# Optimization experiments

Hardware: AMD Instinct MI355X
Metric: run time of the kernel (lower is better)

Reference implementation:

```python
import jax, jax.numpy as jnp
import numpy as np

KE_KCAL = 332.0636  # Coulomb constant, kcal/mol * Angstrom / e^2
R_CUT = 5.0
R_ON = R_CUT / 4.0
R_OFF = 3.0 * R_CUT / 4.0
B, A, F = 32, 1024, 128  # molecules, atoms per molecule, feature dim
MAX_Z = 86


def silu(x):
    return x * jax.nn.sigmoid(x)


def res_mlp(x, W1, W2, Wout):
    # Residual (two pre-activation linears) -> activation -> Linear, no biases
    h = silu(x) @ W1
    h = silu(h) @ W2
    return silu(x + h) @ Wout


def f_switch(r):
    # smooth switching function built from sigma(x)=exp(-1/x) for x>0 else 0
    arg = (r - R_ON) / (R_OFF - R_ON)
    def sigma(x):
        xs = jnp.where(x > 0, x, 1.0)
        return jnp.where(x > 0, jnp.exp(-1.0 / xs), 0.0)
    num = sigma(1.0 - arg)
    return num / (num + sigma(arg))


def setup_inputs() -> dict:
    key = jax.random.key(0)
    ks = jax.random.split(key, 16)
    box = 22.0  # ~liquid density box for 1024 atoms (Angstrom)
    s = 1.0 / np.sqrt(F)
    return {
        'e_z': jax.random.normal(ks[0], (B * A, F), jnp.float32) * 0.1,
        'charge': jax.random.normal(ks[1], (B,), jnp.float32),
        'xyz': jax.random.uniform(ks[2], (B, A, 3), jnp.float32) * box,
        'W_lin': jax.random.normal(ks[3], (F, F), jnp.float32) * s,
        'b_lin': jnp.zeros((F,), jnp.float32),
        'k_plus': jax.random.normal(ks[4], (F,), jnp.float32) * s,
        'k_minus': jax.random.normal(ks[5], (F,), jnp.float32) * s,
        'v_plus': jax.random.normal(ks[6], (F,), jnp.float32) * s,
        'v_minus': jax.random.normal(ks[7], (F,), jnp.float32) * s,
        'Wr1': jax.random.normal(ks[8], (F, F), jnp.float32) * s,
        'Wr2': jax.random.normal(ks[9], (F, F), jnp.float32) * s,
        'Wout': jax.random.normal(ks[10], (F, F), jnp.float32) * s,
        'w_e': jax.random.normal(ks[11], (F,), jnp.float32) * s,
        'q_z_table': jax.random.normal(ks[12], (MAX_Z,), jnp.float32) * 0.01,
        'z': jax.random.randint(ks[13], (B * A,), 1, MAX_Z, jnp.int32),
    }


def reference(e_z, charge, xyz, W_lin, b_lin, k_plus, k_minus, v_plus, v_minus,
              Wr1, Wr2, Wout, w_e, q_z_table, z):
    # ---- ElectronicEmbedding (per-molecule loop vectorized over B) ----
    q = (e_z @ W_lin + b_lin).reshape(B, A, F)
    pos = (charge >= 0)[:, None]                       # [B,1]
    k = jnp.where(pos, k_plus[None, :], k_minus[None, :])   # [B,F]
    v = jnp.where(pos, v_plus[None, :], v_minus[None, :])   # [B,F]
    arg = jnp.einsum('baf,bf->ba', q, k) / np.sqrt(F)
    num = jax.nn.softplus(arg)                         # log(1+exp)
    a = charge[:, None] * num / num.sum(axis=1, keepdims=True)  # [B,A]
    av = a[:, :, None] * v[:, None, :]                 # [B,A,F]
    e_psi = res_mlp(av.reshape(B * A, F), Wr1, Wr2, Wout)
    f = e_z + e_psi                                    # atom features [N,F]

    # ---- Electrostatics.get_charge (charge-conserving correction) ----
    pred_q = (f @ w_e + q_z_table[z]).reshape(B, A)
    corr = (charge - pred_q.sum(axis=1)) / A
    q_atom = pred_q + corr[:, None]                    # [B,A]

    # ---- Electrostatics.get_en: O(A^2) pairwise switched Coulomb ----
    diff = xyz[:, :, None, :] - xyz[:, None, :, :]     # [B,A,A,3]
    r2 = jnp.sum(diff * diff, axis=-1)                 # [B,A,A]
    mask = jnp.triu(jnp.ones((A, A), bool), k=1)       # pairs j > i (r>0)
    r = jnp.sqrt(jnp.where(mask, r2, 1.0))
    fs = f_switch(r)
    coul = fs / jnp.sqrt(r * r + 1.0) + (1.0 - fs) / r
    pair_e = q_atom[:, :, None] * q_atom[:, None, :] * coul
    energy = KE_KCAL * jnp.sum(jnp.where(mask, pair_e, 0.0), axis=(1, 2))  # [B]
    return energy
```

## Files before the change

### kernel.cpp

```cpp
#include <hip/hip_runtime.h>
#include <math.h>

#define B_MOL 32
#define A_AT  1024
#define NF    128
#define N_AT  (B_MOL * A_AT)

#define WS_NUMSUM   512
#define WS_PREDSUM  544
#define WS_PRED     16384
#define WS_SIDX     49152
#define WS_SPOS     81920
#define WS_CTR      214528

typedef short short8 __attribute__((ext_vector_type(8)));
typedef float floatx4 __attribute__((ext_vector_type(4)));

__device__ __forceinline__ float fast_rcp(float x) { return __builtin_amdgcn_rcpf(x); }
__device__ __forceinline__ float fast_rsq(float x) { return __builtin_amdgcn_rsqf(x); }
__device__ __forceinline__ float silu_f(float x) { return x * fast_rcp(1.f + __expf(-x)); }

__device__ __forceinline__ short f2bf(float x) {
  unsigned u = __float_as_uint(x);
  u += 0x7fffu + ((u >> 16) & 1u);
  return (short)(u >> 16);
}

__device__ __forceinline__ float wave_sum(float v) {
#pragma unroll
  for (int o = 32; o > 0; o >>= 1) v += __shfl_xor(v, o, 64);
  return v;
}

__global__ __launch_bounds__(256, 2) void attn_mlp_kernel(
    const float* __restrict__ e_z, const float* __restrict__ charge,
    const float* __restrict__ xyz, const float* __restrict__ W_lin,
    const float* __restrict__ b_lin, const float* __restrict__ k_plus,
    const float* __restrict__ k_minus, const float* __restrict__ v_plus,
    const float* __restrict__ v_minus, const float* __restrict__ Wr1,
    const float* __restrict__ Wr2, const float* __restrict__ Wout,
    const float* __restrict__ w_e, const float* __restrict__ qz_table,
    const int* __restrict__ z, float* __restrict__ ws) {
  int bx = blockIdx.x, tid = threadIdx.x;
  int mol = bx >> 4, s = bx & 15;
  int base = bx * 64;

  __shared__ __align__(16) char big[50176];
  __shared__ float num_sh[64], ezwe_sh[64], wout_sh[128], awsh[64], vsh[128];
  __shared__ float cc_sh, bsum_sh;

  float* k2 = (float*)big;
  float* wesh = k2 + 128;
  int* hist = (int*)(wesh + 128);
  int* startc = hist + 64;
  float* numred = (float*)(startc + 64);
  unsigned* ctr = (unsigned*)(ws + WS_CTR) + mol * 16;

  float ch = charge[mol];
  bool cpos = ch >= 0.f;
  const float* kvec = cpos ? k_plus : k_minus;

  {
    int r = tid & 127;
    const float* M = (tid < 128) ? W_lin : Wout;
    const float* vv = (tid < 128) ? kvec : w_e;
    const float4* row = (const float4*)(M + (size_t)r * NF);
    float acc = 0.f;
#pragma unroll 8
    for (int i = 0; i < 32; i++) {
      float4 a = row[i];
      float4 b = ((const float4*)vv)[i];
      acc = fmaf(a.x, b.x, acc); acc = fmaf(a.y, b.y, acc);
      acc = fmaf(a.z, b.z, acc); acc = fmaf(a.w, b.w, acc);
    }
    if (tid < 128) { k2[r] = acc; wesh[r] = w_e[r]; }
    else wout_sh[r] = acc;
  }
  if (tid < 64) {
    float c = b_lin[tid] * kvec[tid] + b_lin[tid + 64] * kvec[tid + 64];
    c = wave_sum(c);
    if (tid == 0) cc_sh = c;
  }
  __syncthreads();

  int w = tid >> 6, l = tid & 63, half = l >> 5, l31 = l & 31;
  {
    int b4 = l31 * 4;
    float ka = k2[b4], kb = k2[b4 + 1], kc = k2[b4 + 2], kd = k2[b4 + 3];
    float wa = wesh[b4], wb = wesh[b4 + 1], wc = wesh[b4 + 2], wd = wesh[b4 + 3];
    float cc = cc_sh;
    float wavenum = 0.f;
#pragma unroll
    for (int it = 0; it < 8; it++) {
      int m = it * 8 + w * 2 + half;
      int n = base + m;
      float4 v = *((const float4*)(e_z + (size_t)n * NF) + l31);
      float dk = v.x * ka; dk = fmaf(v.y, kb, dk); dk = fmaf(v.z, kc, dk); dk = fmaf(v.w, kd, dk);
      float dw = v.x * wa; dw = fmaf(v.y, wb, dw); dw = fmaf(v.z, wc, dw); dw = fmaf(v.w, wd, dw);
#pragma unroll
      for (int o = 1; o < 32; o <<= 1) {
        dk += __shfl_xor(dk, o, 64);
        dw += __shfl_xor(dw, o, 64);
      }
      if (l31 == 0) {
        float arg = (dk + cc) * 0.08838834764831845f;
        float num = fmaxf(arg, 0.f) + log1pf(__expf(-fabsf(arg)));
        num_sh[m] = num;
        ezwe_sh[m] = dw;
        wavenum += num;
      }
    }
    wavenum += __shfl_xor(wavenum, 32, 64);
    if (l == 0) numred[w] = wavenum;
  }
  __syncthreads();
  if (tid == 0)
    atomicAdd(&ws[WS_NUMSUM + mol], numred[0] + numred[1] + numred[2] + numred[3]);

  if (s == 0) {
    if (tid < 64) hist[tid] = 0;
    __syncthreads();
    float px[4], py[4], pz[4];
    int cell[4];
#pragma unroll
    for (int r = 0; r < 4; r++) {
      int j = tid + r * 256;
      const float* p = xyz + (size_t)(mol * A_AT + j) * 3;
      px[r] = p[0]; py[r] = p[1]; pz[r] = p[2];
      int cx = min(3, max(0, (int)(px[r] * (4.f / 22.f))));
      int cy = min(3, max(0, (int)(py[r] * (4.f / 22.f))));
      int cz = min(3, max(0, (int)(pz[r] * (4.f / 22.f))));
      cell[r] = cx * 16 + cy * 4 + cz;
      atomicAdd(&hist[cell[r]], 1);
    }
    __syncthreads();
    if (tid == 0) {
      int acc = 0;
      for (int c = 0; c < 64; c++) { startc[c] = acc; acc += hist[c]; }
    }
    __syncthreads();
    float4* spos = (float4*)(ws + WS_SPOS);
    int* sidx = (int*)(ws + WS_SIDX);
#pragma unroll
    for (int r = 0; r < 4; r++) {
      int j = tid + r * 256;
      int off = atomicAdd(&startc[cell[r]], 1);
      int g = mol * A_AT + off;
      spos[g] = make_float4(px[r], py[r], pz[r], 0.f);
      sidx[g] = j;
    }
  }

  __syncthreads();
  if (tid == 0) {
    __hip_atomic_fetch_add(ctr, 1u, __ATOMIC_RELAXED, __HIP_MEMORY_SCOPE_AGENT);
    while (__hip_atomic_fetch_add(ctr, 0u, __ATOMIC_RELAXED,
                                  __HIP_MEMORY_SCOPE_AGENT) < 16u)
      __builtin_amdgcn_s_sleep(8);
    bsum_sh = __hip_atomic_fetch_add(&ws[WS_NUMSUM + mol], 0.0f,
                                     __ATOMIC_RELAXED, __HIP_MEMORY_SCOPE_AGENT);
  }
  if (tid < 128) vsh[tid] = cpos ? v_plus[tid] : v_minus[tid];
  __syncthreads();
  if (tid < 64) awsh[tid] = ch * num_sh[tid] / bsum_sh;

  short* wf = (short*)big;
  short* a2s = (short*)(big + 32768);
#pragma unroll
  for (int e = 0; e < 8; e++) {
    int idx = e * 256 + tid;
    int fi = idx >> 6, ln = idx & 63;
    int nt = fi >> 2, ks = fi & 3;
    const float* src = Wr1 + (size_t)(ks * 32 + (ln >> 4) * 8) * NF + nt * 16 + (ln & 15);
    short8 v;
#pragma unroll
    for (int j = 0; j < 8; j++) v[j] = f2bf(src[j * NF]);
    *(short8*)&wf[idx * 8] = v;
  }
  __syncthreads();

  int q = l >> 4, l15 = l & 15;
  float aw_m = awsh[w * 16 + l15];
  floatx4 acc1[8];
#pragma unroll
  for (int nt = 0; nt < 8; nt++) acc1[nt] = (floatx4)(0.f);

#pragma unroll
  for (int ks = 0; ks < 4; ks++) {
    float4 va = *(const float4*)&vsh[ks * 32 + q * 8];
    float4 vb = *(const float4*)&vsh[ks * 32 + q * 8 + 4];
    short8 af;
    af[0] = f2bf(silu_f(aw_m * va.x)); af[1] = f2bf(silu_f(aw_m * va.y));
    af[2] = f2bf(silu_f(aw_m * va.z)); af[3] = f2bf(silu_f(aw_m * va.w));
    af[4] = f2bf(silu_f(aw_m * vb.x)); af[5] = f2bf(silu_f(aw_m * vb.y));
    af[6] = f2bf(silu_f(aw_m * vb.z)); af[7] = f2bf(silu_f(aw_m * vb.w));
#pragma unroll
    for (int nt = 0; nt < 8; nt++) {
      short8 bf = *(const short8*)&wf[(nt * 4 + ks) * 512 + l * 8];
      acc1[nt] = __builtin_amdgcn_mfma_f32_16x16x32_bf16(af, bf, acc1[nt], 0, 0, 0);
    }
  }

#pragma unroll
  for (int nt = 0; nt < 8; nt++) {
    int f = nt * 16 + l15;
#pragma unroll
    for (int r = 0; r < 4; r++)
      a2s[w * 2176 + (q * 4 + r) * 136 + f] = f2bf(silu_f(acc1[nt][r]));
  }
  __syncthreads();
#pragma unroll
  for (int e = 0; e < 8; e++) {
    int idx = e * 256 + tid;
    int fi = idx >> 6, ln = idx & 63;
    int nt = fi >> 2, ks = fi & 3;
    const float* src = Wr2 + (size_t)(ks * 32 + (ln >> 4) * 8) * NF + nt * 16 + (ln & 15);
    short8 v;
#pragma unroll
    for (int j = 0; j < 8; j++) v[j] = f2bf(src[j * NF]);
    *(short8*)&wf[idx * 8] = v;
  }
  __syncthreads();

  floatx4 acc2[8];
#pragma unroll
  for (int nt = 0; nt < 8; nt++) acc2[nt] = (floatx4)(0.f);

#pragma unroll
  for (int ks = 0; ks < 4; ks++) {
    short8 af = *(const short8*)&a2s[w * 2176 + l15 * 136 + ks * 32 + q * 8];
#pragma unroll
    for (int nt = 0; nt < 8; nt++) {
      short8 bf = *(const short8*)&wf[(nt * 4 + ks) * 512 + l * 8];
      acc2[nt] = __builtin_amdgcn_mfma_f32_16x16x32_bf16(af, bf, acc2[nt], 0, 0, 0);
    }
  }

  float awq[4], part[4];
#pragma unroll
  for (int r = 0; r < 4; r++) {
    awq[r] = awsh[w * 16 + q * 4 + r];
    part[r] = 0.f;
  }
#pragma unroll
  for (int nt = 0; nt < 8; nt++) {
    int f = nt * 16 + l15;
    float vv = vsh[f], ww2 = wout_sh[f];
#pragma unroll
    for (int r = 0; r < 4; r++) {
      float sfl = silu_f(fmaf(awq[r], vv, acc2[nt][r]));
      part[r] = fmaf(sfl, ww2, part[r]);
    }
  }
#pragma unroll
  for (int r = 0; r < 4; r++) {
#pragma unroll
    for (int o = 1; o < 16; o <<= 1) part[r] += __shfl_xor(part[r], o, 64);
  }
  float* pred_shf = (float*)(big + 32768);
  __syncthreads();
  if (l15 == 0) {
#pragma unroll
    for (int r = 0; r < 4; r++) {
      int m = w * 16 + q * 4 + r;
      int n = base + m;
      float pred = part[r] + ezwe_sh[m] + qz_table[z[n]];
      ws[WS_PRED + n] = pred;
      pred_shf[m] = pred;
    }
  }
  __syncthreads();
  if (tid < 64) {
    float ssum = wave_sum(pred_shf[tid]);
    if (tid == 0) atomicAdd(&ws[WS_PREDSUM + mol], ssum);
  }
}

__global__ __launch_bounds__(256) void pair_kernel(const float* __restrict__ charge,
                                                   float* __restrict__ ws,
                                                   float* __restrict__ out) {
  int bx = blockIdx.x;
  int mol = bx >> 4;
  int s = bx & 15;
  int tid = threadIdx.x;
  int w = tid >> 6, lane = tid & 63;
  __shared__ float4 posq[1024];
  __shared__ float wred[4];
  const float4* spos = (const float4*)(ws + WS_SPOS);
  const int* sidx = (const int*)(ws + WS_SIDX);
  float corr = (charge[mol] - ws[WS_PREDSUM + mol]) * (1.f / 1024.f);
  for (int j = tid; j < 1024; j += 256) {
    float4 p = spos[mol * 1024 + j];
    p.w = ws[WS_PRED + mol * 1024 + sidx[mol * 1024 + j]] + corr;
    posq[j] = p;
  }
  __syncthreads();
  int i = s * 64 + lane;
  float4 me = posq[i];
  float e = 0.f;
  for (int c = s + w; c < 16; c += 4) {
    int j0 = c * 64;
    if (c == s) {
#pragma unroll 4
      for (int j = j0; j < j0 + 64; j++) {
        float4 p = posq[j];
        float dx = me.x - p.x, dy = me.y - p.y, dz = me.z - p.z;
        float r2 = fmaf(dx, dx, fmaf(dy, dy, dz * dz));
        bool skip = (j <= i);
        float r2s = skip ? 1.0e8f : r2;
        float qj = skip ? 0.f : p.w;
        float inv_r = fast_rsq(r2s);
        e = fmaf(qj, inv_r, e);
        if (__any(r2s < 14.0625f)) {
          float r = r2s * inv_r;
          float arg = (r - 1.25f) * 0.4f;
          float argc = fminf(fmaxf(arg, 1e-6f), 1.f - 1e-6f);
          float t = fast_rcp(argc) - fast_rcp(1.f - argc);
          float fs = fast_rcp(1.f + __expf(-t));
          float delta = fs * (fast_rsq(r2s + 1.f) - inv_r);
          e = fmaf(qj, delta, e);
        }
      }
    } else {
#pragma unroll 4
      for (int j = j0; j < j0 + 64; j++) {
        float4 p = posq[j];
        float dx = me.x - p.x, dy = me.y - p.y, dz = me.z - p.z;
        float r2 = fmaf(dx, dx, fmaf(dy, dy, dz * dz));
        float qj = p.w;
        float inv_r = fast_rsq(r2);
        e = fmaf(qj, inv_r, e);
        if (__any(r2 < 14.0625f)) {
          float r = r2 * inv_r;
          float arg = (r - 1.25f) * 0.4f;
          float argc = fminf(fmaxf(arg, 1e-6f), 1.f - 1e-6f);
          float t = fast_rcp(argc) - fast_rcp(1.f - argc);
          float fs = fast_rcp(1.f + __expf(-t));
          float delta = fs * (fast_rsq(r2 + 1.f) - inv_r);
          e = fmaf(qj, delta, e);
        }
      }
    }
  }
  e *= me.w;
  float sred = wave_sum(e);
  if (lane == 0) wred[w] = sred;
  __syncthreads();
  if (tid == 0)
    atomicAdd(&out[mol], 332.0636f * (wred[0] + wred[1] + wred[2] + wred[3]));
}

extern "C" void kernel_launch(void* const* d_in, const int* in_sizes, int n_in,
                              void* d_out, int out_size, void* d_ws, size_t ws_size,
                              hipStream_t stream) {
  const float* e_z     = (const float*)d_in[0];
  const float* charge  = (const float*)d_in[1];
  const float* xyz     = (const float*)d_in[2];
  const float* W_lin   = (const float*)d_in[3];
  const float* b_lin   = (const float*)d_in[4];
  const float* k_plus  = (const float*)d_in[5];
  const float* k_minus = (const float*)d_in[6];
  const float* v_plus  = (const float*)d_in[7];
  const float* v_minus = (const float*)d_in[8];
  const float* Wr1     = (const float*)d_in[9];
  const float* Wr2     = (const float*)d_in[10];
  const float* Wout    = (const float*)d_in[11];
  const float* w_e     = (const float*)d_in[12];
  const float* qz      = (const float*)d_in[13];
  const int*   z       = (const int*)d_in[14];
  float* out = (float*)d_out;
  float* ws  = (float*)d_ws;

  hipMemsetAsync(ws + WS_NUMSUM, 0, 64 * sizeof(float), stream);
  hipMemsetAsync(ws + WS_CTR, 0, 512 * sizeof(unsigned), stream);
  hipMemsetAsync(out, 0, B_MOL * sizeof(float), stream);
  attn_mlp_kernel<<<512, 256, 0, stream>>>(e_z, charge, xyz, W_lin, b_lin,
                                           k_plus, k_minus, v_plus, v_minus,
                                           Wr1, Wr2, Wout, w_e, qz, z, ws);
  pair_kernel<<<512, 256, 0, stream>>>(charge, ws, out);
}
```

Baseline: 154.3 us.

## Split fused attention/MLP kernel into three launches, drop spin barrier and memsets

Replaces the intra-kernel grid spin-wait (per-molecule counter plus atomic num-sum) with a kernel boundary. A new first kernel computes softplus numerators, sorts atoms into cells and pre-converts Wr1/Wr2 into bf16 MFMA fragment layout once. An MLP kernel then copies those fragments from global memory instead of converting per block. The three memsets are removed (out is zeroed inside the first kernel, sums are recomputed locally), and the pair kernel balances its triangular block work with a rotated chunk schedule. This adds a launch and extra global round-trips for intermediates.

```diff
diff --git a/kernel.cpp b/kernel.cpp
--- a/kernel.cpp
+++ b/kernel.cpp
@@ -6,12 +6,14 @@
 #define NF    128
 #define N_AT  (B_MOL * A_AT)
 
-#define WS_NUMSUM   512
-#define WS_PREDSUM  544
-#define WS_PRED     16384
-#define WS_SIDX     49152
-#define WS_SPOS     81920
-#define WS_CTR      214528
+#define WS_FRAG1    0
+#define WS_FRAG2    8192
+#define WS_WOUT     16384
+#define WS_NUM      16512
+#define WS_EZWE     49280
+#define WS_PREDS    82048
+#define WS_IINV     114816
+#define WS_SPOS     147584
 
 typedef short short8 __attribute__((ext_vector_type(8)));
 typedef float floatx4 __attribute__((ext_vector_type(4)));
@@ -32,49 +34,37 @@
   return v;
 }
 
-__global__ __launch_bounds__(256, 2) void attn_mlp_kernel(
+__global__ __launch_bounds__(256) void attn_sort_kernel(
     const float* __restrict__ e_z, const float* __restrict__ charge,
     const float* __restrict__ xyz, const float* __restrict__ W_lin,
     const float* __restrict__ b_lin, const float* __restrict__ k_plus,
-    const float* __restrict__ k_minus, const float* __restrict__ v_plus,
-    const float* __restrict__ v_minus, const float* __restrict__ Wr1,
+    const float* __restrict__ k_minus, const float* __restrict__ Wr1,
     const float* __restrict__ Wr2, const float* __restrict__ Wout,
-    const float* __restrict__ w_e, const float* __restrict__ qz_table,
-    const int* __restrict__ z, float* __restrict__ ws) {
+    const float* __restrict__ w_e, float* __restrict__ ws,
+    float* __restrict__ out) {
   int bx = blockIdx.x, tid = threadIdx.x;
   int mol = bx >> 4, s = bx & 15;
   int base = bx * 64;
 
-  __shared__ __align__(16) char big[50176];
-  __shared__ float num_sh[64], ezwe_sh[64], wout_sh[128], awsh[64], vsh[128];
-  __shared__ float cc_sh, bsum_sh;
-
-  float* k2 = (float*)big;
-  float* wesh = k2 + 128;
-  int* hist = (int*)(wesh + 128);
-  int* startc = hist + 64;
-  float* numred = (float*)(startc + 64);
-  unsigned* ctr = (unsigned*)(ws + WS_CTR) + mol * 16;
+  __shared__ float k2[NF], wesh[NF];
+  __shared__ int hist[64], startc[64];
+  __shared__ float cc_sh;
 
   float ch = charge[mol];
-  bool cpos = ch >= 0.f;
-  const float* kvec = cpos ? k_plus : k_minus;
-
-  {
-    int r = tid & 127;
-    const float* M = (tid < 128) ? W_lin : Wout;
-    const float* vv = (tid < 128) ? kvec : w_e;
-    const float4* row = (const float4*)(M + (size_t)r * NF);
+  const float* kvec = (ch >= 0.f) ? k_plus : k_minus;
+
+  if (tid < 128) {
+    const float4* row = (const float4*)(W_lin + (size_t)tid * NF);
     float acc = 0.f;
 #pragma unroll 8
     for (int i = 0; i < 32; i++) {
       float4 a = row[i];
-      float4 b = ((const float4*)vv)[i];
+      float4 b = ((const float4*)kvec)[i];
       acc = fmaf(a.x, b.x, acc); acc = fmaf(a.y, b.y, acc);
       acc = fmaf(a.z, b.z, acc); acc = fmaf(a.w, b.w, acc);
     }
-    if (tid < 128) { k2[r] = acc; wesh[r] = w_e[r]; }
-    else wout_sh[r] = acc;
+    k2[tid] = acc;
+    wesh[tid] = w_e[tid];
   }
   if (tid < 64) {
     float c = b_lin[tid] * kvec[tid] + b_lin[tid + 64] * kvec[tid + 64];
@@ -89,7 +79,6 @@
     float ka = k2[b4], kb = k2[b4 + 1], kc = k2[b4 + 2], kd = k2[b4 + 3];
     float wa = wesh[b4], wb = wesh[b4 + 1], wc = wesh[b4 + 2], wd = wesh[b4 + 3];
     float cc = cc_sh;
-    float wavenum = 0.f;
 #pragma unroll
     for (int it = 0; it < 8; it++) {
       int m = it * 8 + w * 2 + half;
@@ -104,18 +93,11 @@
       }
       if (l31 == 0) {
         float arg = (dk + cc) * 0.08838834764831845f;
-        float num = fmaxf(arg, 0.f) + log1pf(__expf(-fabsf(arg)));
-        num_sh[m] = num;
-        ezwe_sh[m] = dw;
-        wavenum += num;
-      }
-    }
-    wavenum += __shfl_xor(wavenum, 32, 64);
-    if (l == 0) numred[w] = wavenum;
-  }
-  __syncthreads();
-  if (tid == 0)
-    atomicAdd(&ws[WS_NUMSUM + mol], numred[0] + numred[1] + numred[2] + numred[3]);
+        ws[WS_NUM + n] = fmaxf(arg, 0.f) + log1pf(__expf(-fabsf(arg)));
+        ws[WS_EZWE + n] = dw;
+      }
+    }
+  }
 
   if (s == 0) {
     if (tid < 64) hist[tid] = 0;
@@ -140,42 +122,80 @@
     }
     __syncthreads();
     float4* spos = (float4*)(ws + WS_SPOS);
-    int* sidx = (int*)(ws + WS_SIDX);
+    int* iinv = (int*)ws + WS_IINV;
 #pragma unroll
     for (int r = 0; r < 4; r++) {
       int j = tid + r * 256;
       int off = atomicAdd(&startc[cell[r]], 1);
-      int g = mol * A_AT + off;
-      spos[g] = make_float4(px[r], py[r], pz[r], 0.f);
-      sidx[g] = j;
-    }
-  }
-
-  __syncthreads();
-  if (tid == 0) {
-    __hip_atomic_fetch_add(ctr, 1u, __ATOMIC_RELAXED, __HIP_MEMORY_SCOPE_AGENT);
-    while (__hip_atomic_fetch_add(ctr, 0u, __ATOMIC_RELAXED,
-                                  __HIP_MEMORY_SCOPE_AGENT) < 16u)
-      __builtin_amdgcn_s_sleep(8);
-    bsum_sh = __hip_atomic_fetch_add(&ws[WS_NUMSUM + mol], 0.0f,
-                                     __ATOMIC_RELAXED, __HIP_MEMORY_SCOPE_AGENT);
-  }
-  if (tid < 128) vsh[tid] = cpos ? v_plus[tid] : v_minus[tid];
-  __syncthreads();
-  if (tid < 64) awsh[tid] = ch * num_sh[tid] / bsum_sh;
-
-  short* wf = (short*)big;
-  short* a2s = (short*)(big + 32768);
-#pragma unroll
-  for (int e = 0; e < 8; e++) {
-    int idx = e * 256 + tid;
-    int fi = idx >> 6, ln = idx & 63;
-    int nt = fi >> 2, ks = fi & 3;
-    const float* src = Wr1 + (size_t)(ks * 32 + (ln >> 4) * 8) * NF + nt * 16 + (ln & 15);
-    short8 v;
-#pragma unroll
-    for (int j = 0; j < 8; j++) v[j] = f2bf(src[j * NF]);
-    *(short8*)&wf[idx * 8] = v;
+      spos[mol * A_AT + off] = make_float4(px[r], py[r], pz[r], 0.f);
+      iinv[mol * A_AT + j] = mol * A_AT + off;
+    }
+  } else if (mol == 0 && (s == 1 || s == 2)) {
+    const float* W = (s == 1) ? Wr1 : Wr2;
+    short* dst = (short*)(ws + ((s == 1) ? WS_FRAG1 : WS_FRAG2));
+#pragma unroll
+    for (int it = 0; it < 16; it++) {
+      int idx = it * 256 + tid;
+      int k = idx >> 5;
+      int c0 = (idx & 31) * 4;
+      float4 v = ((const float4*)W)[idx];
+      int ks = k >> 5, q = (k & 31) >> 3, j = k & 7;
+      float vv[4] = {v.x, v.y, v.z, v.w};
+#pragma unroll
+      for (int e = 0; e < 4; e++) {
+        int col = c0 + e;
+        int fi = (col >> 4) * 4 + ks;
+        int lane = q * 16 + (col & 15);
+        dst[fi * 512 + lane * 8 + j] = f2bf(vv[e]);
+      }
+    }
+  } else if (mol == 0 && s == 3) {
+    if (tid < 128) {
+      float sw = 0.f;
+      for (int f = 0; f < NF; f++) sw = fmaf(Wout[tid * NF + f], w_e[f], sw);
+      ws[WS_WOUT + tid] = sw;
+    }
+    if (tid >= 128 && tid < 160) out[tid - 128] = 0.f;
+  }
+}
+
+__global__ __launch_bounds__(256) void mlp_kernel(
+    const float* __restrict__ charge, const float* __restrict__ v_plus,
+    const float* __restrict__ v_minus, const int* __restrict__ z,
+    const float* __restrict__ qz_table, float* __restrict__ ws) {
+  int bx = blockIdx.x, tid = threadIdx.x;
+  int mol = bx >> 4;
+  int base = bx * 64;
+  int w = tid >> 6, l = tid & 63;
+
+  __shared__ __align__(16) short wf[16384];
+  __shared__ short a2s[4 * 16 * 136];
+  __shared__ float vsh[NF], wout_sh[NF], awsh[64], ezwe_sh[64], wred[4];
+  __shared__ float numsum_sh;
+
+  float ch = charge[mol];
+  {
+    float4 nv = ((const float4*)(ws + WS_NUM + mol * A_AT))[tid];
+    float p = nv.x + nv.y + nv.z + nv.w;
+    p = wave_sum(p);
+    if (l == 0) wred[w] = p;
+  }
+  if (tid < 128) {
+    vsh[tid] = (ch >= 0.f) ? v_plus[tid] : v_minus[tid];
+    wout_sh[tid] = ws[WS_WOUT + tid];
+  }
+  {
+    const float4* src = (const float4*)(ws + WS_FRAG1);
+    float4* dst = (float4*)wf;
+#pragma unroll
+    for (int r = 0; r < 8; r++) dst[tid + r * 256] = src[tid + r * 256];
+  }
+  __syncthreads();
+  if (tid == 0) numsum_sh = wred[0] + wred[1] + wred[2] + wred[3];
+  __syncthreads();
+  if (tid < 64) {
+    awsh[tid] = ch * ws[WS_NUM + base + tid] / numsum_sh;
+    ezwe_sh[tid] = ws[WS_EZWE + base + tid];
   }
   __syncthreads();
 
@@ -209,16 +229,11 @@
       a2s[w * 2176 + (q * 4 + r) * 136 + f] = f2bf(silu_f(acc1[nt][r]));
   }
   __syncthreads();
-#pragma unroll
-  for (int e = 0; e < 8; e++) {
-    int idx = e * 256 + tid;
-    int fi = idx >> 6, ln = idx & 63;
-    int nt = fi >> 2, ks = fi & 3;
-    const float* src = Wr2 + (size_t)(ks * 32 + (ln >> 4) * 8) * NF + nt * 16 + (ln & 15);
-    short8 v;
-#pragma unroll
-    for (int j = 0; j < 8; j++) v[j] = f2bf(src[j * NF]);
-    *(short8*)&wf[idx * 8] = v;
+  {
+    const float4* src = (const float4*)(ws + WS_FRAG2);
+    float4* dst = (float4*)wf;
+#pragma unroll
+    for (int r = 0; r < 8; r++) dst[tid + r * 256] = src[tid + r * 256];
   }
   __syncthreads();
 
@@ -257,50 +272,52 @@
 #pragma unroll
     for (int o = 1; o < 16; o <<= 1) part[r] += __shfl_xor(part[r], o, 64);
   }
-  float* pred_shf = (float*)(big + 32768);
-  __syncthreads();
   if (l15 == 0) {
+    const int* iinv = (const int*)ws + WS_IINV;
 #pragma unroll
     for (int r = 0; r < 4; r++) {
       int m = w * 16 + q * 4 + r;
       int n = base + m;
-      float pred = part[r] + ezwe_sh[m] + qz_table[z[n]];
-      ws[WS_PRED + n] = pred;
-      pred_shf[m] = pred;
-    }
-  }
-  __syncthreads();
-  if (tid < 64) {
-    float ssum = wave_sum(pred_shf[tid]);
-    if (tid == 0) atomicAdd(&ws[WS_PREDSUM + mol], ssum);
+      ws[WS_PREDS + iinv[n]] = part[r] + ezwe_sh[m] + qz_table[z[n]];
+    }
   }
 }
 
 __global__ __launch_bounds__(256) void pair_kernel(const float* __restrict__ charge,
-                                                   float* __restrict__ ws,
+                                                   const float* __restrict__ ws,
                                                    float* __restrict__ out) {
   int bx = blockIdx.x;
   int mol = bx >> 4;
-  int s = bx & 15;
+  int a = bx & 15;
   int tid = threadIdx.x;
-  int w = tid >> 6, lane = tid & 63;
+  int w = tid >> 6, l = tid & 63;
   __shared__ float4 posq[1024];
   __shared__ float wred[4];
   const float4* spos = (const float4*)(ws + WS_SPOS);
-  const int* sidx = (const int*)(ws + WS_SIDX);
-  float corr = (charge[mol] - ws[WS_PREDSUM + mol]) * (1.f / 1024.f);
+  const float* preds = ws + WS_PREDS + mol * A_AT;
+  float psum = 0.f;
   for (int j = tid; j < 1024; j += 256) {
-    float4 p = spos[mol * 1024 + j];
-    p.w = ws[WS_PRED + mol * 1024 + sidx[mol * 1024 + j]] + corr;
+    float4 p = spos[mol * A_AT + j];
+    p.w = preds[j];
     posq[j] = p;
-  }
-  __syncthreads();
-  int i = s * 64 + lane;
+    psum += p.w;
+  }
+  psum = wave_sum(psum);
+  if (l == 0) wred[w] = psum;
+  __syncthreads();
+  float corr = (charge[mol] - (wred[0] + wred[1] + wred[2] + wred[3])) * (1.f / 1024.f);
+  for (int j = tid; j < 1024; j += 256) posq[j].w += corr;
+  __syncthreads();
+
+  int i = a * 64 + l;
   float4 me = posq[i];
   float e = 0.f;
-  for (int c = s + w; c < 16; c += 4) {
+#pragma unroll
+  for (int t = 0; t < 2; t++) {
+    int d = w + t * 4;
+    int c = (a + d) & 15;
     int j0 = c * 64;
-    if (c == s) {
+    if (d == 0) {
 #pragma unroll 4
       for (int j = j0; j < j0 + 64; j++) {
         float4 p = posq[j];
@@ -315,8 +332,8 @@
           float r = r2s * inv_r;
           float arg = (r - 1.25f) * 0.4f;
           float argc = fminf(fmaxf(arg, 1e-6f), 1.f - 1e-6f);
-          float t = fast_rcp(argc) - fast_rcp(1.f - argc);
-          float fs = fast_rcp(1.f + __expf(-t));
+          float tt = fast_rcp(argc) - fast_rcp(1.f - argc);
+          float fs = fast_rcp(1.f + __expf(-tt));
           float delta = fs * (fast_rsq(r2s + 1.f) - inv_r);
           e = fmaf(qj, delta, e);
         }
@@ -334,17 +351,38 @@
           float r = r2 * inv_r;
           float arg = (r - 1.25f) * 0.4f;
           float argc = fminf(fmaxf(arg, 1e-6f), 1.f - 1e-6f);
-          float t = fast_rcp(argc) - fast_rcp(1.f - argc);
-          float fs = fast_rcp(1.f + __expf(-t));
+          float tt = fast_rcp(argc) - fast_rcp(1.f - argc);
+          float fs = fast_rcp(1.f + __expf(-tt));
           float delta = fs * (fast_rsq(r2 + 1.f) - inv_r);
           e = fmaf(qj, delta, e);
         }
       }
     }
   }
+  if (a < 8 && w == (a & 3)) {
+    int j0 = ((a + 8) & 15) * 64;
+#pragma unroll 4
+    for (int j = j0; j < j0 + 64; j++) {
+      float4 p = posq[j];
+      float dx = me.x - p.x, dy = me.y - p.y, dz = me.z - p.z;
+      float r2 = fmaf(dx, dx, fmaf(dy, dy, dz * dz));
+      float qj = p.w;
+      float inv_r = fast_rsq(r2);
+      e = fmaf(qj, inv_r, e);
+      if (__any(r2 < 14.0625f)) {
+        float r = r2 * inv_r;
+        float arg = (r - 1.25f) * 0.4f;
+        float argc = fminf(fmaxf(arg, 1e-6f), 1.f - 1e-6f);
+        float tt = fast_rcp(argc) - fast_rcp(1.f - argc);
+        float fs = fast_rcp(1.f + __expf(-tt));
+        float delta = fs * (fast_rsq(r2 + 1.f) - inv_r);
+        e = fmaf(qj, delta, e);
+      }
+    }
+  }
   e *= me.w;
   float sred = wave_sum(e);
-  if (lane == 0) wred[w] = sred;
+  if (l == 0) wred[w] = sred;
   __syncthreads();
   if (tid == 0)
     atomicAdd(&out[mol], 332.0636f * (wred[0] + wred[1] + wred[2] + wred[3]));
@@ -371,11 +409,9 @@
   float* out = (float*)d_out;
   float* ws  = (float*)d_ws;
 
-  hipMemsetAsync(ws + WS_NUMSUM, 0, 64 * sizeof(float), stream);
-  hipMemsetAsync(ws + WS_CTR, 0, 512 * sizeof(unsigned), stream);
-  hipMemsetAsync(out, 0, B_MOL * sizeof(float), stream);
-  attn_mlp_kernel<<<512, 256, 0, stream>>>(e_z, charge, xyz, W_lin, b_lin,
-                                           k_plus, k_minus, v_plus, v_minus,
-                                           Wr1, Wr2, Wout, w_e, qz, z, ws);
+  attn_sort_kernel<<<512, 256, 0, stream>>>(e_z, charge, xyz, W_lin, b_lin,
+                                            k_plus, k_minus, Wr1, Wr2, Wout,
+                                            w_e, ws, out);
+  mlp_kernel<<<512, 256, 0, stream>>>(charge, v_plus, v_minus, z, qz, ws);
   pair_kernel<<<512, 256, 0, stream>>>(charge, ws, out);
 }
```

After: 136.8 us. 11.4% less time.
